# Kernel tuning notes

Hardware: AMD Instinct MI355X
Metric: run time of the kernel (lower is better)

The kernel has to match this reference:

```python
import jax, jax.numpy as jnp
import numpy as np
from jax import lax

B, C, H, W = 128, 512, 10, 20
MD, S2 = 20, 2  # max_displacement, stride2 -> 21x21 = 441 displacements


def setup_inputs() -> dict:
    key = jax.random.key(0)
    ks = jax.random.split(key, 26)
    rn = lambda k, s, sc: jax.random.normal(k, s, jnp.float32) * sc
    z = lambda s: jnp.zeros(s, jnp.float32)
    return {
        "feat1": rn(ks[0], (B, C, H, W), 1.0),
        "feat2": rn(ks[1], (B, C, H, W), 1.0),
        "feat3": rn(ks[2], (B, C, H, W), 1.0),
        # 1x1 input convs
        "Wa": rn(ks[3], (512, 512), 0.001), "ba": z(512),
        "Wb": rn(ks[4], (512, 512), 0.001), "bb": z(512),
        "Wc": rn(ks[5], (512, 512), 0.001), "bc": z(512),
        # corr head 3x3 conv: 441*3 -> 3
        "Wcorr": rn(ks[6], (3, 1323, 3, 3), 0.001), "bcorr": z(3),
        # concat head 3x3 conv: 1536 -> 3
        "Wcat": rn(ks[7], (3, 1536, 3, 3), 0.001), "bcat": z(3),
        # corr_feat MLP 600->256->128
        "cf_w1": rn(ks[8], (256, 600), 0.01), "cf_b1": z(256),
        "cf_w2": rn(ks[9], (128, 256), 0.01), "cf_b2": z(128),
        # concat_feat MLP 600->256->128
        "ccf_w1": rn(ks[10], (256, 600), 0.01), "ccf_b1": z(256),
        "ccf_w2": rn(ks[11], (128, 256), 0.01), "ccf_b2": z(128),
        # final linear 256->2
        "Wout": rn(ks[12], (2, 256), 0.01), "bout": z(2),
    }


def _conv1x1(x, w, b):
    return jnp.einsum('bchw,oc->bohw', x, w) + b[None, :, None, None]


def _conv3x3(x, w, b):
    y = lax.conv_general_dilated(x, w, (1, 1), 'SAME',
                                 dimension_numbers=('NCHW', 'OIHW', 'NCHW'))
    return y + b[None, :, None, None]


def _correlation(f1, f2):
    # FlowNetC-style cost volume: pad_size=20, kernel_size=1,
    # max_displacement=20, stride1=1, stride2=2 -> 21x21=441 channels,
    # normalized by C (kernel_size^2 * C with kernel_size=1).
    p = jnp.pad(f2, ((0, 0), (0, 0), (MD, MD), (MD, MD)))
    outs = []
    for dy in range(0, 2 * MD + 1, S2):
        for dx in range(0, 2 * MD + 1, S2):
            outs.append(jnp.sum(f1 * p[:, :, dy:dy + H, dx:dx + W], axis=1))
    return jnp.stack(outs, axis=1) / f1.shape[1]  # [B, 441, H, W]


def reference(feat1, feat2, feat3, Wa, ba, Wb, bb, Wc, bc,
              Wcorr, bcorr, Wcat, bcat,
              cf_w1, cf_b1, cf_w2, cf_b2,
              ccf_w1, ccf_b1, ccf_w2, ccf_b2, Wout, bout):
    f1 = _conv1x1(feat1, Wa, ba)
    f2 = _conv1x1(feat2, Wb, bb)
    f3 = _conv1x1(feat3, Wc, bc)

    corr = jnp.concatenate([_correlation(f1, f2),
                            _correlation(f1, f3),
                            _correlation(f2, f3)], axis=1)  # [B,1323,H,W]
    corr = jax.nn.leaky_relu(corr, 0.1)
    corr = jax.nn.relu(_conv3x3(corr, Wcorr, bcorr))  # [B,3,H,W]
    corr = corr.reshape(corr.shape[0], -1)            # [B,600]
    corr = jax.nn.relu(corr @ cf_w1.T + cf_b1)
    corr = jax.nn.relu(corr @ cf_w2.T + cf_b2)        # [B,128]

    cat = jnp.concatenate([f1, f2, f3], axis=1)       # [B,1536,H,W]
    cat = _conv3x3(cat, Wcat, bcat)                   # [B,3,H,W] (no relu, per source)
    cat = cat.reshape(cat.shape[0], -1)               # [B,600]
    cat = jax.nn.relu(cat @ ccf_w1.T + ccf_b1)
    cat = jax.nn.relu(cat @ ccf_w2.T + ccf_b2)        # [B,128]

    out = jnp.concatenate([corr, cat], axis=1)        # [B,256]
    return out @ Wout.T + bout                        # [B,2]
```

## Files before the change

kernel.cpp:

```cpp
#include <hip/hip_runtime.h>
#include <stdint.h>

#define NB 128
#define NC 512
#define NH 10
#define NW 20
#define NP 200
#define ND3 1323
#define NDP 448
#define MROWS 25600
#define KCORR 1344
#define KCAT  1536

typedef unsigned short u16;
typedef unsigned int u32;

typedef short bh8 __attribute__((ext_vector_type(8)));
typedef float f4 __attribute__((ext_vector_type(4)));

#define OFF_FA     0ULL
#define SZ_FA      (3ULL*MROWS*NC*2)
#define OFF_CORR   0ULL
#define SZ_CORR    (3ULL*NB*NP*NDP*2)
#define OFF_UCORR  (OFF_CORR + SZ_CORR + 256)
#define SZ_U       (1ULL*MROWS*32*4)
#define OFF_UCAT   (OFF_UCORR + SZ_U)
#define OFF_FT     (OFF_FA + SZ_FA)
#define SZ_FT      (3ULL*MROWS*NC*2 + 65536)
#define OFF_WBF    (OFF_FT + SZ_FT)
#define SZ_WBF     (3ULL*NC*NC*2)
#define OFF_WCTB   (OFF_WBF + SZ_WBF)
#define SZ_WCTB    (32ULL*KCORR*2)
#define OFF_WCATB  (OFF_WCTB + SZ_WCTB)
#define SZ_WCATB   (32ULL*KCAT*2)

__device__ __forceinline__ float bf2f(u16 a) {
    return __uint_as_float(((u32)a) << 16);
}
__device__ __forceinline__ u16 f2bf(float x) {
    u32 u = __float_as_uint(x);
    return (u16)((u + 0x7fffu + ((u >> 16) & 1u)) >> 16);
}

__device__ __forceinline__ void gload16(const void* g, void* l) {
    __builtin_amdgcn_global_load_lds(
        (const __attribute__((address_space(1))) void*)g,
        (__attribute__((address_space(3))) void*)l, 16, 0, 0);
}

__global__ __launch_bounds__(256) void k_prep_fa(
    const float* __restrict__ feat1, const float* __restrict__ feat2,
    const float* __restrict__ feat3, u16* __restrict__ fa,
    const float* __restrict__ Wcorr, const float* __restrict__ Wcat,
    const float* __restrict__ Wa, const float* __restrict__ Wb,
    const float* __restrict__ Wc, u16* __restrict__ wctb,
    u16* __restrict__ wcatb, u16* __restrict__ wbf) {
    const int tid = threadIdx.x;
    const int bid = blockIdx.x;
    if (bid < 3072) {
        const int ct = bid & 7;
        const int yy = bid >> 3;
        const int t = yy >> 7, b = yy & 127;
        const float* feat = (t == 0) ? feat1 : (t == 1) ? feat2 : feat3;

        __shared__ u16 Ls[NP * 72];

        const int cl = tid >> 2;
        const int pc = tid & 3;
        const float* src = feat + ((size_t)b * NC + ct * 64 + cl) * NP + pc * 50;
#pragma unroll
        for (int u = 0; u < 50; u += 2) {
            float2 v = *(const float2*)(src + u);
            int p = pc * 50 + u;
            Ls[p * 72 + cl] = f2bf(v.x);
            Ls[(p + 1) * 72 + cl] = f2bf(v.y);
        }
        __syncthreads();
        for (int idx = tid; idx < 1600; idx += 256) {
            int p = idx >> 3, ck = idx & 7;
            uint4 v = *(const uint4*)&Ls[p * 72 + ck * 8];
            *(uint4*)&fa[((size_t)t * MROWS + b * NP + p) * NC + ct * 64 + ck * 8] = v;
        }
    } else {
        int idx = (bid - 3072) * 256 + tid;
        const int n1 = 32 * KCORR;
        const int n2 = 32 * KCAT;
        const int n3 = 3 * NC * NC;
        if (idx < n1) {
            int k = idx % KCORR;
            int n = idx / KCORR;
            int pair = k / NDP, ch = k - pair * NDP;
            float v = 0.0f;
            if (n < 27 && ch < 441) {
                int d = pair * 441 + ch;
                int tap = n / 3, o = n % 3;
                int ky = tap / 3, kx = tap % 3;
                v = Wcorr[((o * ND3 + d) * 3 + ky) * 3 + kx];
            }
            wctb[idx] = f2bf(v);
        } else if (idx < n1 + n2) {
            int j = idx - n1;
            int i = j % KCAT;
            int n = j / KCAT;
            float v = 0.0f;
            if (n < 27) {
                int tap = n / 3, o = n % 3;
                int ky = tap / 3, kx = tap % 3;
                v = Wcat[((o * 1536 + i) * 3 + ky) * 3 + kx];
            }
            wcatb[j] = f2bf(v);
        } else if (idx < n1 + n2 + n3) {
            int j = idx - n1 - n2;
            int t = j >> 18;
            const float* W = (t == 0) ? Wa : (t == 1) ? Wb : Wc;
            wbf[j] = f2bf(W[j & 262143]);
        }
    }
}

__global__ __launch_bounds__(256) void k_conv1x1_mfma(
    const u16* __restrict__ fa, const u16* __restrict__ wbf,
    const float* __restrict__ ba, const float* __restrict__ bb,
    const float* __restrict__ bc, u16* __restrict__ fT) {
    const int tid = threadIdx.x;
    const int bid = blockIdx.x;
    const int xcd = bid & 7, local = bid >> 3;
    const int mb = xcd * 25 + local / 12;
    const int nbt = local % 12;
    const int nb = nbt & 3;
    const int t = nbt >> 2;
    const float* bias = (t == 0) ? ba : (t == 1) ? bb : bc;

    __shared__ __align__(16) u16 smem[17408];

    const u16* Ag = fa + (size_t)t * MROWS * NC + (size_t)mb * 128 * NC;
    const u16* Bg = wbf + (size_t)t * NC * NC + (size_t)nb * 128 * NC;

    const int lane = tid & 63;
    const int wave = tid >> 6;
    const int wm = (wave & 1) * 64;
    const int wn = (wave >> 1) * 64;
    const int quad = lane >> 4;
    const int ln16 = lane & 15;

    const int rL = lane >> 2;
    const int csrc = (lane & 3) ^ ((lane >> 2) & 3) ^ ((lane >> 4) & 3);
    const int qs = (quad ^ (ln16 & 3) ^ ((ln16 >> 2) & 3)) * 8;

    float bi[4];
#pragma unroll
    for (int j = 0; j < 4; ++j) bi[j] = bias[nb * 128 + wn + j * 16 + ln16];
    asm volatile("s_waitcnt vmcnt(0)" ::: "memory");
    __builtin_amdgcn_sched_barrier(0);

    f4 acc[4][4];
    const f4 zz = {0.f, 0.f, 0.f, 0.f};
#pragma unroll
    for (int i = 0; i < 4; ++i)
#pragma unroll
        for (int j = 0; j < 4; ++j) acc[i][j] = zz;

#define STAGE1(buf, ks) do {                                                   \
        int _ko = (ks) * 32 + csrc * 8;                                        \
        _Pragma("unroll")                                                      \
        for (int _i = 0; _i < 2; ++_i) {                                       \
            int _c = wave * 2 + _i;                                            \
            gload16(Ag + (size_t)(16 * _c + rL) * NC + _ko,                    \
                    &smem[(buf) * 4096 + _c * 512]);                           \
            gload16(Bg + (size_t)(16 * _c + rL) * NC + _ko,                    \
                    &smem[8192 + (buf) * 4096 + _c * 512]);                    \
        }                                                                      \
    } while (0)

    STAGE1(0, 0);
    STAGE1(1, 1);
#pragma unroll
    for (int ks = 0; ks < 16; ++ks) {
        if (ks < 15) asm volatile("s_waitcnt vmcnt(4)" ::: "memory");
        else         asm volatile("s_waitcnt vmcnt(0)" ::: "memory");
        __builtin_amdgcn_s_barrier();
        __builtin_amdgcn_sched_barrier(0);
        {
            const u16* Ab = &smem[(ks & 1) * 4096];
            const u16* Bb = &smem[8192 + (ks & 1) * 4096];
            bh8 afr[4], bfr[4];
#pragma unroll
            for (int s = 0; s < 4; ++s) {
                afr[s] = *(const bh8*)&Ab[(wm + s * 16 + ln16) * 32 + qs];
                bfr[s] = *(const bh8*)&Bb[(wn + s * 16 + ln16) * 32 + qs];
            }
#pragma unroll
            for (int i = 0; i < 4; ++i)
#pragma unroll
                for (int j = 0; j < 4; ++j)
                    acc[i][j] = __builtin_amdgcn_mfma_f32_16x16x32_bf16(
                        afr[i], bfr[j], acc[i][j], 0, 0, 0);
        }
        __builtin_amdgcn_sched_barrier(0);
        __builtin_amdgcn_s_barrier();
        __builtin_amdgcn_sched_barrier(0);
        if (ks < 14) STAGE1(ks & 1, ks + 2);
    }
#undef STAGE1

    __syncthreads();
#pragma unroll
    for (int j = 0; j < 4; ++j) {
        int tcol = wn + j * 16 + ln16;
#pragma unroll
        for (int i = 0; i < 4; ++i) {
            int trow = wm + i * 16 + quad * 4;
#pragma unroll
            for (int r = 0; r < 4; ++r)
                smem[(trow + r) * 136 + tcol] = f2bf(acc[i][j][r] + bi[j]);
        }
    }
    __syncthreads();
    const size_t obase = ((size_t)t * MROWS + (size_t)mb * 128) * NC + nb * 128;
#pragma unroll
    for (int it = 0; it < 8; ++it) {
        int idx = tid + 256 * it;
        int row = idx >> 4, ck = idx & 15;
        *(uint4*)(fT + obase + (size_t)row * NC + ck * 8) =
            *(const uint4*)&smem[row * 136 + ck * 8];
    }
}

__global__ __launch_bounds__(256) void k_gram_mfma(const u16* __restrict__ fT,
                                                   u16* __restrict__ corr) {
    const int tid = threadIdx.x;
    const int bid = blockIdx.x;
    const int xcd = bid & 7, local = bid >> 3;
    const int gidx = xcd * 48 + (local >> 2);
    const int mt = local & 3;
    const int b = gidx / 3, pair = gidx % 3;
    const int tA = (pair == 2) ? 1 : 0;
    const int tB = (pair == 0) ? 1 : 2;

    __shared__ __align__(16) u16 smem[20480];

    const u16* Ag = fT + ((size_t)tA * NB + b) * NP * NC + (size_t)mt * 64 * NC;
    const u16* Bg = fT + ((size_t)tB * NB + b) * NP * NC;

    const int lane = tid & 63;
    const int wave = tid >> 6;
    const int wn = wave * 64;
    const int quad = lane >> 4;
    const int ln16 = lane & 15;

    const int r0 = lane >> 3;
    const int csrc = (lane & 7) ^ r0;

    f4 acc[4][4];
    const f4 zz = {0.f, 0.f, 0.f, 0.f};
#pragma unroll
    for (int i = 0; i < 4; ++i)
#pragma unroll
        for (int j = 0; j < 4; ++j) acc[i][j] = zz;

#define STAGE2(ks) do {                                                        \
        int _ko = (ks) * 64 + csrc * 8;                                        \
        _Pragma("unroll")                                                      \
        for (int _i = 0; _i < 2; ++_i) {                                       \
            int _ra = wave * 16 + _i * 8;                                      \
            gload16(Ag + (size_t)(_ra + r0) * NC + _ko, &smem[_ra * 64]);      \
        }                                                                      \
        _Pragma("unroll")                                                      \
        for (int _i = 0; _i < 8; ++_i) {                                       \
            int _rb = wave * 64 + _i * 8;                                      \
            gload16(Bg + (size_t)(_rb + r0) * NC + _ko,                        \
                    &smem[4096 + _rb * 64]);                                   \
        }                                                                      \
    } while (0)

#pragma unroll
    for (int ks = 0; ks < 8; ++ks) {
        __syncthreads();
        STAGE2(ks);
        __syncthreads();
#pragma unroll
        for (int h = 0; h < 2; ++h) {
            bh8 afr[4], bfr[4];
#pragma unroll
            for (int s = 0; s < 4; ++s) {
                int cw = ((h * 4 + quad) ^ (ln16 & 7)) * 8;
                afr[s] = *(const bh8*)&smem[(s * 16 + ln16) * 64 + cw];
                bfr[s] = *(const bh8*)&smem[4096 + (wn + s * 16 + ln16) * 64 + cw];
            }
#pragma unroll
            for (int i = 0; i < 4; ++i)
#pragma unroll
                for (int j = 0; j < 4; ++j)
                    acc[i][j] = __builtin_amdgcn_mfma_f32_16x16x32_bf16(
                        afr[i], bfr[j], acc[i][j], 0, 0, 0);
        }
    }
#undef STAGE2

    u16* Crow = corr + ((size_t)(b * 3 + pair)) * NP * NDP;
#pragma unroll
    for (int half = 0; half < 2; ++half) {
        __syncthreads();
        {
            const uint4 z4 = make_uint4(0, 0, 0, 0);
#pragma unroll
            for (int it = 0; it < 14; ++it)
                ((uint4*)smem)[tid + 256 * it] = z4;
        }
        __syncthreads();
#pragma unroll
        for (int i = half * 2; i < half * 2 + 2; ++i) {
#pragma unroll
            for (int r = 0; r < 4; ++r) {
                int p1l = i * 16 + quad * 4 + r;
                int lrow = p1l - half * 32;
                int p1 = mt * 64 + p1l;
                if (p1 >= NP) continue;
                int y1 = p1 / 20, x1 = p1 - y1 * 20;
#pragma unroll
                for (int j = 0; j < 4; ++j) {
                    int p2 = wn + j * 16 + ln16;
                    if (p2 >= NP) continue;
                    int y2 = p2 / 20, x2 = p2 - y2 * 20;
                    int oy = y2 - y1, ox = x2 - x1;
                    if (((oy | ox) & 1) == 0) {
                        int ch = ((oy + 20) >> 1) * 21 + ((ox + 20) >> 1);
                        float v = acc[i][j][r] * (1.0f / 512.0f);
                        v = (v > 0.0f) ? v : 0.1f * v;
                        smem[lrow * NDP + ch] = f2bf(v);
                    }
                }
            }
        }
        __syncthreads();
#pragma unroll
        for (int it = 0; it < 7; ++it) {
            int idx = tid + 256 * it;
            int row = idx / 56, cq = idx - row * 56;
            int p1 = mt * 64 + half * 32 + row;
            if (p1 < NP)
                *(uint4*)(Crow + (size_t)p1 * NDP + cq * 8) =
                    *(const uint4*)&smem[row * NDP + cq * 8];
        }
    }
}

__global__ __launch_bounds__(256) void k_convgemm(const u16* __restrict__ corr,
                                                  const u16* __restrict__ fT,
                                                  const u16* __restrict__ wctb,
                                                  const u16* __restrict__ wcatb,
                                                  float* __restrict__ Ucorr,
                                                  float* __restrict__ Ucat) {
    const int tid = threadIdx.x;
    const int mode = blockIdx.y;
    const u16* A0 = mode ? fT : corr;
    const u16* Bn = mode ? wcatb : wctb;
    float* U = mode ? Ucat : Ucorr;
    const int kiters = mode ? (KCAT / 64) : (KCORR / 64);
    const int Kpad = kiters * 64;

    const int lane = tid & 63;
    const int wave = tid >> 6;
    const int quad = lane >> 4;
    const int ln16 = lane & 15;
    const int wbase = (blockIdx.x * 4 + wave) * 16;
    const int arow = wbase + ln16;

    size_t abase;
    if (mode == 0) {
        int b = arow / NP, p = arow - b * NP;
        abase = ((size_t)(b * 3) * NP + p) * NDP;
    } else {
        abase = (size_t)arow * NC;
    }

    f4 acc0 = {0, 0, 0, 0}, acc1 = {0, 0, 0, 0};

    bh8 pa[2][2], pb0[2][2], pb1[2][2];

#define PFC(buf, ks) do {                                                      \
        _Pragma("unroll")                                                      \
        for (int _h = 0; _h < 2; ++_h) {                                       \
            int _k = (ks) * 64 + _h * 32 + quad * 8;                           \
            const u16* _ap;                                                    \
            if (mode == 0) {                                                   \
                int _pr = _k / NDP;                                            \
                _ap = A0 + abase + (size_t)_pr * (NP * NDP) + (_k - _pr * NDP);\
            } else {                                                           \
                _ap = A0 + (size_t)(_k >> 9) * ((size_t)MROWS * NC) + abase    \
                      + (_k & 511);                                            \
            }                                                                  \
            pa[buf][_h]  = *(const bh8*)_ap;                                   \
            pb0[buf][_h] = *(const bh8*)(Bn + (size_t)ln16 * Kpad + _k);       \
            pb1[buf][_h] = *(const bh8*)(Bn + (size_t)(16 + ln16) * Kpad + _k);\
        }                                                                      \
    } while (0)

#define CGM(buf) do {                                                          \
        acc0 = __builtin_amdgcn_mfma_f32_16x16x32_bf16(pa[buf][0],             \
                   pb0[buf][0], acc0, 0, 0, 0);                                \
        acc1 = __builtin_amdgcn_mfma_f32_16x16x32_bf16(pa[buf][0],             \
                   pb1[buf][0], acc1, 0, 0, 0);                                \
        acc0 = __builtin_amdgcn_mfma_f32_16x16x32_bf16(pa[buf][1],             \
                   pb0[buf][1], acc0, 0, 0, 0);                                \
        acc1 = __builtin_amdgcn_mfma_f32_16x16x32_bf16(pa[buf][1],             \
                   pb1[buf][1], acc1, 0, 0, 0);                                \
    } while (0)

    PFC(0, 0);
    PFC(1, 1);
    int ks = 0;
    for (; ks + 1 < kiters; ks += 2) {
        CGM(0);
        if (ks + 2 < kiters) PFC(0, ks + 2);
        CGM(1);
        if (ks + 3 < kiters) PFC(1, ks + 3);
    }
    if (ks < kiters) CGM(0);
#undef PFC
#undef CGM

    const int orow = wbase + quad * 4;
#pragma unroll
    for (int r = 0; r < 4; ++r) {
        U[(size_t)(orow + r) * 32 + ln16] = acc0[r];
        U[(size_t)(orow + r) * 32 + 16 + ln16] = acc1[r];
    }
}

__global__ __launch_bounds__(256) void k_tail(
    const float* __restrict__ Ucorr, const float* __restrict__ Ucat,
    const float* __restrict__ bcorr, const float* __restrict__ bcat,
    const float* __restrict__ cf_w1, const float* __restrict__ cf_b1,
    const float* __restrict__ cf_w2, const float* __restrict__ cf_b2,
    const float* __restrict__ ccf_w1, const float* __restrict__ ccf_b1,
    const float* __restrict__ ccf_w2, const float* __restrict__ ccf_b2,
    const float* __restrict__ Wout, const float* __restrict__ bout,
    float* __restrict__ out) {
    const int tid = threadIdx.x;
    const int b = blockIdx.x;
    __shared__ float Lc[NP][28];
    __shared__ float La[NP][28];
    __shared__ float cv[600], vv[600], h1[256], h2a[128], h2b[128];
    for (int idx = tid; idx < NP * 27; idx += 256) {
        int p = idx / 27, n = idx - p * 27;
        Lc[p][n] = Ucorr[(size_t)(b * NP + p) * 32 + n];
        La[p][n] = Ucat[(size_t)(b * NP + p) * 32 + n];
    }
    __syncthreads();
    for (int idx = tid; idx < 1200; idx += 256) {
        int path = idx / 600;
        int rem = idx - path * 600;
        int o = rem / 200, p = rem - o * 200;
        int y = p / 20, x = p - y * 20;
        float s = (path == 0) ? bcorr[o] : bcat[o];
        for (int ky = 0; ky < 3; ++ky) {
            int yy = y + ky - 1;
            if (yy < 0 || yy >= NH) continue;
            for (int kx = 0; kx < 3; ++kx) {
                int xx = x + kx - 1;
                if (xx < 0 || xx >= NW) continue;
                int n = (ky * 3 + kx) * 3 + o;
                s += (path == 0) ? Lc[yy * 20 + xx][n] : La[yy * 20 + xx][n];
            }
        }
        if (path == 0) cv[rem] = fmaxf(s, 0.0f);
        else           vv[rem] = s;
    }
    __syncthreads();
    {
        float s = cf_b1[tid];
        const float* wr = cf_w1 + (size_t)tid * 600;
        for (int k = 0; k < 600; k += 4) {
            float4 wv = *(const float4*)&wr[k];
            s = fmaf(cv[k], wv.x, s); s = fmaf(cv[k + 1], wv.y, s);
            s = fmaf(cv[k + 2], wv.z, s); s = fmaf(cv[k + 3], wv.w, s);
        }
        h1[tid] = fmaxf(s, 0.0f);
    }
    __syncthreads();
    if (tid < 128) {
        float s = cf_b2[tid];
        const float* wr = cf_w2 + (size_t)tid * 256;
        for (int k = 0; k < 256; k += 4) {
            float4 wv = *(const float4*)&wr[k];
            s = fmaf(h1[k], wv.x, s); s = fmaf(h1[k + 1], wv.y, s);
            s = fmaf(h1[k + 2], wv.z, s); s = fmaf(h1[k + 3], wv.w, s);
        }
        h2a[tid] = fmaxf(s, 0.0f);
    }
    __syncthreads();
    {
        float s = ccf_b1[tid];
        const float* wr = ccf_w1 + (size_t)tid * 600;
        for (int k = 0; k < 600; k += 4) {
            float4 wv = *(const float4*)&wr[k];
            s = fmaf(vv[k], wv.x, s); s = fmaf(vv[k + 1], wv.y, s);
            s = fmaf(vv[k + 2], wv.z, s); s = fmaf(vv[k + 3], wv.w, s);
        }
        h1[tid] = fmaxf(s, 0.0f);
    }
    __syncthreads();
    if (tid < 128) {
        float s = ccf_b2[tid];
        const float* wr = ccf_w2 + (size_t)tid * 256;
        for (int k = 0; k < 256; k += 4) {
            float4 wv = *(const float4*)&wr[k];
            s = fmaf(h1[k], wv.x, s); s = fmaf(h1[k + 1], wv.y, s);
            s = fmaf(h1[k + 2], wv.z, s); s = fmaf(h1[k + 3], wv.w, s);
        }
        h2b[tid] = fmaxf(s, 0.0f);
    }
    __syncthreads();
    if (tid < 2) {
        float s = bout[tid];
        const float* wr = Wout + (size_t)tid * 256;
        for (int k = 0; k < 128; ++k) {
            s = fmaf(h2a[k], wr[k], s);
            s = fmaf(h2b[k], wr[128 + k], s);
        }
        out[(size_t)b * 2 + tid] = s;
    }
}

extern "C" void kernel_launch(void* const* d_in, const int* in_sizes, int n_in,
                              void* d_out, int out_size, void* d_ws, size_t ws_size,
                              hipStream_t stream) {
    const float* feat1  = (const float*)d_in[0];
    const float* feat2  = (const float*)d_in[1];
    const float* feat3  = (const float*)d_in[2];
    const float* Wa     = (const float*)d_in[3];
    const float* ba     = (const float*)d_in[4];
    const float* Wb     = (const float*)d_in[5];
    const float* bb     = (const float*)d_in[6];
    const float* Wc     = (const float*)d_in[7];
    const float* bc     = (const float*)d_in[8];
    const float* Wcorr  = (const float*)d_in[9];
    const float* bcorr  = (const float*)d_in[10];
    const float* Wcat   = (const float*)d_in[11];
    const float* bcat   = (const float*)d_in[12];
    const float* cf_w1  = (const float*)d_in[13];
    const float* cf_b1  = (const float*)d_in[14];
    const float* cf_w2  = (const float*)d_in[15];
    const float* cf_b2  = (const float*)d_in[16];
    const float* ccf_w1 = (const float*)d_in[17];
    const float* ccf_b1 = (const float*)d_in[18];
    const float* ccf_w2 = (const float*)d_in[19];
    const float* ccf_b2 = (const float*)d_in[20];
    const float* Wout   = (const float*)d_in[21];
    const float* bout   = (const float*)d_in[22];

    char* ws = (char*)d_ws;
    u16*  fa    = (u16*)(ws + OFF_FA);
    u16*  corr  = (u16*)(ws + OFF_CORR);
    float* Ucorr = (float*)(ws + OFF_UCORR);
    float* Ucat  = (float*)(ws + OFF_UCAT);
    u16*  fT    = (u16*)(ws + OFF_FT);
    u16*  wbf   = (u16*)(ws + OFF_WBF);
    u16*  wctb  = (u16*)(ws + OFF_WCTB);
    u16*  wcatb = (u16*)(ws + OFF_WCATB);

    k_prep_fa<<<6504, 256, 0, stream>>>(feat1, feat2, feat3, fa,
                                        Wcorr, Wcat, Wa, Wb, Wc,
                                        wctb, wcatb, wbf);
    k_conv1x1_mfma<<<2400, 256, 0, stream>>>(fa, wbf, ba, bb, bc, fT);
    k_gram_mfma<<<1536, 256, 0, stream>>>(fT, corr);
    k_convgemm<<<dim3(400, 2), 256, 0, stream>>>(corr, fT, wctb, wcatb, Ucorr, Ucat);
    k_tail<<<128, 256, 0, stream>>>(Ucorr, Ucat, bcorr, bcat,
                                    cf_w1, cf_b1, cf_w2, cf_b2,
                                    ccf_w1, ccf_b1, ccf_w2, ccf_b2, Wout, bout,
                                    (float*)d_out);
}
```

Measured before the change: 447.4 us.

## Double-buffer correlation GEMM K-loop with async loads and widen transpose reads

The correlation GEMM's K loop changes from 8 single-buffered 64-wide steps, each with two full barriers, to 16 double-buffered 32-wide steps. Direct-to-LDS loads for step k+2 are issued while step k computes, with explicit vmcnt waits and sched barriers, and the LDS swizzle is redone for the 32-element rows. The input transpose kernel also switches from float2 to float4 global reads. The aim is to hide global load latency behind MFMA work, at the cost of fragile hand-tuned waitcnt counts.

After: 437.2 us. 2.3% less time.

```diff
diff --git a/kernel.cpp b/kernel.cpp
--- a/kernel.cpp
+++ b/kernel.cpp
@@ -67,13 +67,23 @@
 
         const int cl = tid >> 2;
         const int pc = tid & 3;
-        const float* src = feat + ((size_t)b * NC + ct * 64 + cl) * NP + pc * 50;
-#pragma unroll
-        for (int u = 0; u < 50; u += 2) {
-            float2 v = *(const float2*)(src + u);
-            int p = pc * 50 + u;
-            Ls[p * 72 + cl] = f2bf(v.x);
+        const float* src = feat + ((size_t)b * NC + ct * 64 + cl) * NP;
+#pragma unroll
+        for (int u = 0; u < 12; ++u) {
+            int p = u * 16 + pc * 4;
+            float4 v = *(const float4*)(src + p);
+            Ls[(p + 0) * 72 + cl] = f2bf(v.x);
             Ls[(p + 1) * 72 + cl] = f2bf(v.y);
+            Ls[(p + 2) * 72 + cl] = f2bf(v.z);
+            Ls[(p + 3) * 72 + cl] = f2bf(v.w);
+        }
+        if (pc < 2) {
+            int p = 192 + pc * 4;
+            float4 v = *(const float4*)(src + p);
+            Ls[(p + 0) * 72 + cl] = f2bf(v.x);
+            Ls[(p + 1) * 72 + cl] = f2bf(v.y);
+            Ls[(p + 2) * 72 + cl] = f2bf(v.z);
+            Ls[(p + 3) * 72 + cl] = f2bf(v.w);
         }
         __syncthreads();
         for (int idx = tid; idx < 1600; idx += 256) {
@@ -248,8 +258,9 @@
     const int quad = lane >> 4;
     const int ln16 = lane & 15;
 
-    const int r0 = lane >> 3;
-    const int csrc = (lane & 7) ^ r0;
+    const int rL = lane >> 2;
+    const int csrc = (lane & 3) ^ ((lane >> 2) & 3) ^ ((lane >> 4) & 3);
+    const int qs = (quad ^ (ln16 & 3) ^ ((ln16 >> 2) & 3)) * 8;
 
     f4 acc[4][4];
     const f4 zz = {0.f, 0.f, 0.f, 0.f};
@@ -258,34 +269,34 @@
 #pragma unroll
         for (int j = 0; j < 4; ++j) acc[i][j] = zz;
 
-#define STAGE2(ks) do {                                                        \
-        int _ko = (ks) * 64 + csrc * 8;                                        \
+#define STAGE2(buf, ks) do {                                                   \
+        int _ko = (ks) * 32 + csrc * 8;                                        \
+        gload16(Ag + (size_t)(wave * 16 + rL) * NC + _ko,                      \
+                &smem[(buf) * 2048 + wave * 512]);                             \
         _Pragma("unroll")                                                      \
-        for (int _i = 0; _i < 2; ++_i) {                                       \
-            int _ra = wave * 16 + _i * 8;                                      \
-            gload16(Ag + (size_t)(_ra + r0) * NC + _ko, &smem[_ra * 64]);      \
-        }                                                                      \
-        _Pragma("unroll")                                                      \
-        for (int _i = 0; _i < 8; ++_i) {                                       \
-            int _rb = wave * 64 + _i * 8;                                      \
-            gload16(Bg + (size_t)(_rb + r0) * NC + _ko,                        \
-                    &smem[4096 + _rb * 64]);                                   \
+        for (int _i = 0; _i < 4; ++_i) {                                       \
+            int _rb = wave * 64 + _i * 16;                                     \
+            gload16(Bg + (size_t)(_rb + rL) * NC + _ko,                        \
+                    &smem[4096 + (buf) * 8192 + _rb * 32]);                    \
         }                                                                      \
     } while (0)
 
-#pragma unroll
-    for (int ks = 0; ks < 8; ++ks) {
-        __syncthreads();
-        STAGE2(ks);
-        __syncthreads();
-#pragma unroll
-        for (int h = 0; h < 2; ++h) {
+    STAGE2(0, 0);
+    STAGE2(1, 1);
+#pragma unroll
+    for (int ks = 0; ks < 16; ++ks) {
+        if (ks < 15) asm volatile("s_waitcnt vmcnt(5)" ::: "memory");
+        else         asm volatile("s_waitcnt vmcnt(0)" ::: "memory");
+        __builtin_amdgcn_s_barrier();
+        __builtin_amdgcn_sched_barrier(0);
+        {
+            const u16* Ab = &smem[(ks & 1) * 2048];
+            const u16* Bb = &smem[4096 + (ks & 1) * 8192];
             bh8 afr[4], bfr[4];
 #pragma unroll
             for (int s = 0; s < 4; ++s) {
-                int cw = ((h * 4 + quad) ^ (ln16 & 7)) * 8;
-                afr[s] = *(const bh8*)&smem[(s * 16 + ln16) * 64 + cw];
-                bfr[s] = *(const bh8*)&smem[4096 + (wn + s * 16 + ln16) * 64 + cw];
+                afr[s] = *(const bh8*)&Ab[(s * 16 + ln16) * 32 + qs];
+                bfr[s] = *(const bh8*)&Bb[(wn + s * 16 + ln16) * 32 + qs];
             }
 #pragma unroll
             for (int i = 0; i < 4; ++i)
@@ -294,6 +305,10 @@
                     acc[i][j] = __builtin_amdgcn_mfma_f32_16x16x32_bf16(
                         afr[i], bfr[j], acc[i][j], 0, 0, 0);
         }
+        __builtin_amdgcn_sched_barrier(0);
+        __builtin_amdgcn_s_barrier();
+        __builtin_amdgcn_sched_barrier(0);
+        if (ks < 14) STAGE2(ks & 1, ks + 2);
     }
 #undef STAGE2
 
```
